# Optimization experiments

Measured on AMD Instinct MI355X. Metric: run time of the kernel, lower is better.

The kernel has to match this reference:

```python
import jax, jax.numpy as jnp
import numpy as np

B, S, D, H = 2, 2048, 1024, 16
DK = D // H


def setup_inputs() -> dict:
    key = jax.random.key(0)
    ks = jax.random.split(key, 12)
    s = 0.02
    return {
        "q": jax.random.normal(ks[0], (B, S, D), jnp.float32),
        "k": jax.random.normal(ks[1], (B, S, D), jnp.float32),
        "v": jax.random.normal(ks[2], (B, S, D), jnp.float32),
        "mask": jax.random.randint(ks[3], (1, 1, S, S), 0, 2, jnp.int32),
        "Wq": jax.random.normal(ks[4], (D, D), jnp.float32) * s,
        "bq": jnp.zeros((D,), jnp.float32),
        "Wk": jax.random.normal(ks[5], (D, D), jnp.float32) * s,
        "bk": jnp.zeros((D,), jnp.float32),
        "Wv": jax.random.normal(ks[6], (D, D), jnp.float32) * s,
        "bv": jnp.zeros((D,), jnp.float32),
        "Wo": jax.random.normal(ks[7], (D, D), jnp.float32) * s,
        "bo": jnp.zeros((D,), jnp.float32),
    }


def reference(q, k, v, mask, Wq, bq, Wk, bk, Wv, bv, Wo, bo):
    # linear projections (torch Linear: x @ W.T + b)
    qp = q @ Wq.T + bq
    kp = k @ Wk.T + bk
    vp = v @ Wv.T + bv
    # [B, S, D] -> [B, H, S, DK]
    split = lambda x: x.reshape(B, S, H, DK).transpose(0, 2, 1, 3)
    qh, kh, vh = split(qp), split(kp), split(vp)
    scale = 1.0 / jnp.sqrt(jnp.float32(DK))
    attn = jnp.einsum('bhsd,bhtd->bhst', qh, kh) * scale  # [B,H,S,S]
    attn = jnp.where(mask == 0, jnp.float32(-1e9), attn)
    attn = jax.nn.softmax(attn, axis=-1)
    out = jnp.einsum('bhst,bhtd->bhsd', attn, vh)  # [B,H,S,DK]
    concat = out.transpose(0, 2, 1, 3).reshape(B, S, D)
    return concat @ Wo.T + bo
```

## Files before the change

### kernel.cpp

```cpp
#include <hip/hip_runtime.h>
#include <hip/hip_bf16.h>


using bf16x8 = __attribute__((ext_vector_type(8))) short;
using f32x4  = __attribute__((ext_vector_type(4))) float;

constexpr int Bc = 2, Sc = 2048, Dc = 1024, Hc = 16, DKc = 64;
constexpr int Mc = Bc * Sc;
#define QSCALE 0.18033688011112042f

__device__ __forceinline__ void lds_load16(const void* g, void* l) {
  __builtin_amdgcn_global_load_lds(
      (const __attribute__((address_space(1))) unsigned int*)g,
      (__attribute__((address_space(3))) unsigned int*)l, 16, 0, 0);
}

#if __has_builtin(__builtin_amdgcn_exp2f)
__device__ __forceinline__ float exp2_fast(float x) { return __builtin_amdgcn_exp2f(x); }
#else
__device__ __forceinline__ float exp2_fast(float x) {
  float r;
  asm("v_exp_f32 %0, %1\n\ts_nop 0" : "=v"(r) : "v"(x));
  return r;
}
#endif

__device__ __forceinline__ unsigned pack_trunc(float a, float b) {
  return __builtin_amdgcn_perm(__float_as_uint(b), __float_as_uint(a), 0x07060302u);
}

__device__ __forceinline__ unsigned pack2bf(float a, float b) {
  union { __hip_bfloat16 h; unsigned short s; } ua, ub;
  ua.h = __float2bfloat16(a);
  ub.h = __float2bfloat16(b);
  return (unsigned)ua.s | ((unsigned)ub.s << 16);
}

__global__ void prep(const float* __restrict__ q, const float* __restrict__ k,
                     const float* __restrict__ v, const int* __restrict__ mask,
                     const float* __restrict__ Wq, const float* __restrict__ Wk,
                     const float* __restrict__ Wv, const float* __restrict__ Wo,
                     char* __restrict__ ws) {
  const size_t MB = 1024 * 1024;
  int blk = blockIdx.x;
  if (blk < 12288) {
    int which = blk >> 12;
    int i = (((blk & 4095) << 8) + threadIdx.x) * 4;
    const float* s = which == 0 ? q : (which == 1 ? k : v);
    __hip_bfloat16* d = (__hip_bfloat16*)(ws + (size_t)which * 8 * MB);
    float4 x = *(const float4*)&s[i];
    uint2 pk = {pack2bf(x.x, x.y), pack2bf(x.z, x.w)};
    *(uint2*)&d[i] = pk;
  } else if (blk < 16384) {
    int bb = blk - 12288;
    int which = bb >> 10;
    int i = (((bb & 1023) << 8) + threadIdx.x) * 4;
    const float* s = which == 0 ? Wq : (which == 1 ? Wk : (which == 2 ? Wv : Wo));
    __hip_bfloat16* d = which < 3 ? (__hip_bfloat16*)(ws + (24 + 2 * which) * MB)
                                  : (__hip_bfloat16*)(ws + 32 * MB);
    float4 x = *(const float4*)&s[i];
    uint2 pk = {pack2bf(x.x, x.y), pack2bf(x.z, x.w)};
    *(uint2*)&d[i] = pk;
  } else {
    int i = ((blk - 16384) << 8) + threadIdx.x;
    unsigned long long bal = __ballot(mask[i] != 0);
    if ((threadIdx.x & 63) == 0)
      ((unsigned long long*)(ws + 34 * MB))[i >> 6] = bal;
  }
}

__global__ __launch_bounds__(256, 3) void proj_qkv(
    const __hip_bfloat16* __restrict__ qb, const __hip_bfloat16* __restrict__ kb,
    const __hip_bfloat16* __restrict__ vb, const __hip_bfloat16* __restrict__ Wcat,
    const float* __restrict__ bq, const float* __restrict__ bk,
    const float* __restrict__ bv, __hip_bfloat16* __restrict__ qhd,
    __hip_bfloat16* __restrict__ khd, __hip_bfloat16* __restrict__ vtd) {
  __shared__ __align__(16) __hip_bfloat16 As[128 * 64];
  __shared__ __align__(16) __hip_bfloat16 Bs[128 * 64];
  const int tid = threadIdx.x;
  const int f = blockIdx.x, g = f >> 3;
  const int m0 = ((f & 7) * 4 + g / 24) * 128;
  const int n0 = (g % 24) * 128;
  const int which = n0 >> 10, nl0 = n0 & 1023;
  const __hip_bfloat16* X = which == 0 ? qb : (which == 1 ? kb : vb);
  const float* bias = which == 0 ? bq : (which == 1 ? bk : bv);
  const int w = tid >> 6, lane = tid & 63, ln = lane & 15, quad = lane >> 4;
  const int swz = ((lane & 7) ^ (lane >> 3)) * 8;
  const int rk0 = ln * 128 + ((quad ^ (ln & 7)) * 16);
  const int rk1 = ln * 128 + (((quad + 4) ^ (ln & 7)) * 16);
  const int aoff = (m0 + w * 32 + (lane >> 3)) * 1024 + swz;
  const int boff = (n0 + w * 32 + (lane >> 3)) * 1024 + swz;
  char* aF = (char*)As + (w >> 1) * 8192;
  char* bF = (char*)Bs + (w & 1) * 8192;
  char* aDst = (char*)As + w * 4096 + lane * 16;
  char* bDst = (char*)Bs + w * 4096 + lane * 16;
  f32x4 acc[4][4] = {};
  int ko = 0;
  for (int kb64 = 0; kb64 < 16; ++kb64, ko += 64) {
#pragma unroll
    for (int i = 0; i < 4; ++i) {
      lds_load16(&X[aoff + i * 8192 + ko], aDst + i * 1024);
      lds_load16(&Wcat[boff + i * 8192 + ko], bDst + i * 1024);
    }
    __syncthreads();
    bf16x8 af[4][2], bf[4][2];
#pragma unroll
    for (int i = 0; i < 4; ++i) {
      af[i][0] = *(bf16x8*)(aF + i * 2048 + rk0);
      af[i][1] = *(bf16x8*)(aF + i * 2048 + rk1);
      bf[i][0] = *(bf16x8*)(bF + i * 2048 + rk0);
      bf[i][1] = *(bf16x8*)(bF + i * 2048 + rk1);
    }
#pragma unroll
    for (int i = 0; i < 4; ++i)
#pragma unroll
      for (int j = 0; j < 4; ++j) {
        acc[i][j] = __builtin_amdgcn_mfma_f32_16x16x32_bf16(af[i][0], bf[j][0],
                                                            acc[i][j], 0, 0, 0);
        acc[i][j] = __builtin_amdgcn_mfma_f32_16x16x32_bf16(af[i][1], bf[j][1],
                                                            acc[i][j], 0, 0, 0);
      }
    __syncthreads();
  }
  const int wm = (w >> 1) * 64, wn = (w & 1) * 64;
#pragma unroll
  for (int i = 0; i < 4; ++i)
#pragma unroll
    for (int j = 0; j < 4; ++j) {
      int ngl = nl0 + wn + j * 16 + ln;
      int mbase = m0 + wm + i * 16 + quad * 4;
      float bb = bias[ngl];
      float vv[4];
#pragma unroll
      for (int r = 0; r < 4; ++r) vv[r] = acc[i][j][r] + bb;
      int h = ngl >> 6, dk = ngl & 63;
      int b = mbase >> 11, s = mbase & 2047;
      if (which == 0) {
#pragma unroll
        for (int r = 0; r < 4; ++r)
          qhd[(((size_t)(b * Hc + h) * Sc + s + r) * DKc) + dk] =
              __float2bfloat16(vv[r] * QSCALE);
      } else if (which == 1) {
#pragma unroll
        for (int r = 0; r < 4; ++r)
          khd[(((size_t)(b * Hc + h) * Sc + s + r) * DKc) + dk] =
              __float2bfloat16(vv[r]);
      } else {
        uint2 pk = {pack2bf(vv[0], vv[1]), pack2bf(vv[2], vv[3])};
        *(uint2*)&vtd[(((size_t)(b * Hc + h) * DKc + dk) * Sc) + s] = pk;
      }
    }
}

__global__ __launch_bounds__(256, 2) void gemm_out(
    const __hip_bfloat16* __restrict__ X, const __hip_bfloat16* __restrict__ W,
    const float* __restrict__ bias, float* __restrict__ Y) {
  __shared__ __align__(16) __hip_bfloat16 As[2][128 * 64];
  __shared__ __align__(16) __hip_bfloat16 Bs[2][64 * 64];
  const int tid = threadIdx.x;
  const int f = blockIdx.x, g = f >> 3;
  const int m0 = ((f & 7) * 4 + (g >> 4)) * 128;
  const int n0 = (g & 15) * 64;
  const int w = tid >> 6, lane = tid & 63, ln = lane & 15, quad = lane >> 4;
  const int wm = (w >> 1) * 64, wn = (w & 1) * 32;
  const int swz = ((lane & 7) ^ (lane >> 3)) * 8;
  const int rk0 = ln * 128 + ((quad ^ (ln & 7)) * 16);
  const int rk1 = ln * 128 + (((quad + 4) ^ (ln & 7)) * 16);
  const int aoff = (m0 + w * 32 + (lane >> 3)) * 1024 + swz;
  const int boff = (n0 + w * 16 + (lane >> 3)) * 1024 + swz;
  f32x4 acc[4][2] = {};

#define OSTAGE(KO, BI)                                                        \
  {                                                                           \
    _Pragma("unroll") for (int i = 0; i < 4; ++i)                             \
        lds_load16(&X[aoff + i * 8192 + (KO)],                                \
                   (char*)As[BI] + w * 4096 + lane * 16 + i * 1024);          \
    _Pragma("unroll") for (int i = 0; i < 2; ++i)                             \
        lds_load16(&W[boff + i * 8192 + (KO)],                                \
                   (char*)Bs[BI] + w * 2048 + lane * 16 + i * 1024);          \
  }

  OSTAGE(0, 0);
  for (int kb64 = 0; kb64 < 16; ++kb64) {
    const int bi = kb64 & 1;
    __syncthreads();
    if (kb64 + 1 < 16) OSTAGE((kb64 + 1) * 64, bi ^ 1);
    bf16x8 af[4][2], bf[2][2];
#pragma unroll
    for (int i = 0; i < 4; ++i) {
      af[i][0] = *(bf16x8*)((char*)As[bi] + wm * 128 + i * 2048 + rk0);
      af[i][1] = *(bf16x8*)((char*)As[bi] + wm * 128 + i * 2048 + rk1);
    }
#pragma unroll
    for (int j = 0; j < 2; ++j) {
      bf[j][0] = *(bf16x8*)((char*)Bs[bi] + wn * 128 + j * 2048 + rk0);
      bf[j][1] = *(bf16x8*)((char*)Bs[bi] + wn * 128 + j * 2048 + rk1);
    }
#pragma unroll
    for (int i = 0; i < 4; ++i)
#pragma unroll
      for (int j = 0; j < 2; ++j) {
        acc[i][j] = __builtin_amdgcn_mfma_f32_16x16x32_bf16(af[i][0], bf[j][0],
                                                            acc[i][j], 0, 0, 0);
        acc[i][j] = __builtin_amdgcn_mfma_f32_16x16x32_bf16(af[i][1], bf[j][1],
                                                            acc[i][j], 0, 0, 0);
      }
  }
#pragma unroll
  for (int i = 0; i < 4; ++i)
#pragma unroll
    for (int j = 0; j < 2; ++j) {
      int ng = n0 + wn + j * 16 + ln;
      int mbase = m0 + wm + i * 16 + quad * 4;
      float bb = bias[ng];
#pragma unroll
      for (int r = 0; r < 4; ++r)
        Y[(size_t)(mbase + r) * Dc + ng] = acc[i][j][r] + bb;
    }
}

__global__ __launch_bounds__(256, 3) void flash_attn(
    const __hip_bfloat16* __restrict__ qh, const __hip_bfloat16* __restrict__ kh,
    const __hip_bfloat16* __restrict__ vt, const uint4* __restrict__ mb4,
    float* __restrict__ opart, float* __restrict__ lpart) {
  __shared__ __align__(16) char L[51200];
  const int tid = threadIdx.x;
  const int f = blockIdx.x, g = f >> 3;
  const int bhh = (f & 7) * 8 + (g >> 4);
  const int q0 = (g & 15) * 128;
  const int half = bhh >> 5, bh = bhh & 31;
  const int w = tid >> 6, lane = tid & 63, ln = lane & 15, quad = lane >> 4;
  const size_t base = (size_t)bh * Sc * DKc;
  const __hip_bfloat16* khb = kh + base + half * 65536;
  const __hip_bfloat16* vtb = vt + base;

  bf16x8 qf[2][2];
#pragma unroll
  for (int qt = 0; qt < 2; ++qt)
#pragma unroll
    for (int kc = 0; kc < 2; ++kc)
      qf[qt][kc] = *(const bf16x8*)&qh[base +
          (size_t)(q0 + w * 32 + qt * 16 + ln) * 64 + kc * 32 + quad * 8];

  bf16x8 onesA;
#pragma unroll
  for (int i = 0; i < 8; ++i) onesA[i] = (short)0x3F80;

  const int swz = ((lane & 7) ^ (lane >> 3)) * 8;
  const int rk0 = ln * 128 + ((quad ^ (ln & 7)) * 16);
  const int rk1 = ln * 128 + (((quad + 4) ^ (ln & 7)) * 16);
  const int rPw = 32768 + w * 4608 + ln * 144 + quad * 8;
  const int rPb = 32768 + w * 4608 + ln * 144 + quad * 16;
  char* dmaL = L + w * 2048 + lane * 16;
  int koff = (w * 16 + (lane >> 3)) * 64 + swz;
  int voff0 = (w * 16 + (lane >> 3)) * Sc + swz + half * 1024;
  int voff1 = voff0 + 8 * Sc;
  int midx0 = (q0 + w * 32 + ln) * 16 + half * 8;
  int midx1 = midx0 + 256;
  const int sh0 = quad * 4, sh1 = quad * 4 + 16;

#define KV_DMA(BI)                                                            \
  {                                                                           \
    lds_load16(khb + koff, dmaL + (BI)*8192);                                 \
    lds_load16(khb + koff + 512, dmaL + (BI)*8192 + 1024);                    \
    lds_load16(vtb + voff0, dmaL + 16384 + (BI)*8192);                        \
    lds_load16(vtb + voff1, dmaL + 16384 + (BI)*8192 + 1024);                 \
  }

  f32x4 Oacc[4][2] = {};
  f32x4 lacc[2] = {};
  KV_DMA(0);

#define FTILE(BUF, LO0, HI0, LO1, HI1)                                        \
  {                                                                           \
    bf16x8 kf[4][2];                                                          \
    _Pragma("unroll") for (int tt = 0; tt < 4; ++tt) {                        \
      kf[tt][0] = *(bf16x8*)(L + (BUF)*8192 + tt * 2048 + rk0);               \
      kf[tt][1] = *(bf16x8*)(L + (BUF)*8192 + tt * 2048 + rk1);               \
    }                                                                         \
    _Pragma("unroll") for (int qt = 0; qt < 2; ++qt) {                        \
      f32x4 s[4];                                                             \
      _Pragma("unroll") for (int tt = 0; tt < 4; ++tt) {                      \
        f32x4 z = {0.f, 0.f, 0.f, 0.f};                                       \
        z = __builtin_amdgcn_mfma_f32_16x16x32_bf16(kf[tt][0], qf[qt][0], z,  \
                                                    0, 0, 0);                 \
        s[tt] = __builtin_amdgcn_mfma_f32_16x16x32_bf16(kf[tt][1], qf[qt][1], \
                                                        z, 0, 0, 0);          \
      }                                                                       \
      unsigned lo = qt ? (LO1) : (LO0), hi = qt ? (HI1) : (HI0);              \
      _Pragma("unroll") for (int tt = 0; tt < 4; ++tt) {                      \
        unsigned word = (tt & 2) ? hi : lo;                                   \
        unsigned pre = word >> ((tt & 1) ? sh1 : sh0);                        \
        float p[4];                                                           \
        _Pragma("unroll") for (int r = 0; r < 4; ++r) {                       \
          float e = exp2_fast(s[tt][r]);                                      \
          p[r] = (pre & (1u << r)) ? e : 0.f;                                 \
        }                                                                     \
        uint2 pk = {pack_trunc(p[0], p[1]), pack_trunc(p[2], p[3])};          \
        *(uint2*)(L + rPw + qt * 2304 + tt * 32) = pk;                        \
      }                                                                       \
    }                                                                         \
    bf16x8 vf[4][2], pb[2][2];                                                \
    _Pragma("unroll") for (int dt = 0; dt < 4; ++dt) {                        \
      vf[dt][0] = *(bf16x8*)(L + 16384 + (BUF)*8192 + dt * 2048 + rk0);       \
      vf[dt][1] = *(bf16x8*)(L + 16384 + (BUF)*8192 + dt * 2048 + rk1);       \
    }                                                                         \
    _Pragma("unroll") for (int qt = 0; qt < 2; ++qt) {                        \
      pb[qt][0] = *(bf16x8*)(L + rPb + qt * 2304);                            \
      pb[qt][1] = *(bf16x8*)(L + rPb + qt * 2304 + 64);                       \
    }                                                                         \
    _Pragma("unroll") for (int qt = 0; qt < 2; ++qt) {                        \
      lacc[qt] = __builtin_amdgcn_mfma_f32_16x16x32_bf16(onesA, pb[qt][0],    \
                                                         lacc[qt], 0, 0, 0);  \
      lacc[qt] = __builtin_amdgcn_mfma_f32_16x16x32_bf16(onesA, pb[qt][1],    \
                                                         lacc[qt], 0, 0, 0);  \
    }                                                                         \
    _Pragma("unroll") for (int dt = 0; dt < 4; ++dt)                          \
        _Pragma("unroll") for (int qt = 0; qt < 2; ++qt) {                    \
      Oacc[dt][qt] = __builtin_amdgcn_mfma_f32_16x16x32_bf16(                 \
          vf[dt][0], pb[qt][0], Oacc[dt][qt], 0, 0, 0);                       \
      Oacc[dt][qt] = __builtin_amdgcn_mfma_f32_16x16x32_bf16(                 \
          vf[dt][1], pb[qt][1], Oacc[dt][qt], 0, 0, 0);                       \
    }                                                                         \
  }

  for (int it2 = 0; it2 < 8; ++it2) {
    __syncthreads();
    uint4 mq0 = mb4[midx0], mq1 = mb4[midx1];
    ++midx0; ++midx1;
    koff += 4096; voff0 += 64; voff1 += 64;
    KV_DMA(1);
    FTILE(0, mq0.x, mq0.y, mq1.x, mq1.y);
    __syncthreads();
    if (it2 < 7) {
      koff += 4096; voff0 += 64; voff1 += 64;
      KV_DMA(0);
    }
    FTILE(1, mq0.z, mq0.w, mq1.z, mq1.w);
  }

  const size_t obase = (size_t)(half * 32 + bh) * 2048;
#pragma unroll
  for (int qt = 0; qt < 2; ++qt) {
    int qrow = q0 + w * 32 + qt * 16 + ln;
#pragma unroll
    for (int dt = 0; dt < 4; ++dt) {
      f32x4 o = Oacc[dt][qt];
      float4 st = {o[0], o[1], o[2], o[3]};
      *(float4*)&opart[(obase + qrow) * 64 + dt * 16 + quad * 4] = st;
    }
    if (quad == 0) lpart[obase + qrow] = lacc[qt][0];
  }
}

__global__ void reduce_o(const float* __restrict__ opart,
                         const float* __restrict__ lpart,
                         __hip_bfloat16* __restrict__ oc) {
  int t = blockIdx.x * 256 + threadIdx.x;
  int r = t >> 3, dk8 = (t & 7) * 8;
  const size_t HS = (size_t)32 * 2048 * 64;
  float4 a0 = *(const float4*)&opart[(size_t)r * 64 + dk8];
  float4 a1 = *(const float4*)&opart[(size_t)r * 64 + dk8 + 4];
  float4 b0 = *(const float4*)&opart[HS + (size_t)r * 64 + dk8];
  float4 b1 = *(const float4*)&opart[HS + (size_t)r * 64 + dk8 + 4];
  float li = 1.f / fmaxf(lpart[r] + lpart[65536 + r], 1e-30f);
  int bh = r >> 11, qq = r & 2047, b = bh >> 4, h = bh & 15;
  uint4 o;
  o.x = pack2bf((a0.x + b0.x) * li, (a0.y + b0.y) * li);
  o.y = pack2bf((a0.z + b0.z) * li, (a0.w + b0.w) * li);
  o.z = pack2bf((a1.x + b1.x) * li, (a1.y + b1.y) * li);
  o.w = pack2bf((a1.z + b1.z) * li, (a1.w + b1.w) * li);
  *(uint4*)&oc[((size_t)(b * Sc + qq) * Dc) + h * 64 + dk8] = o;
}

extern "C" void kernel_launch(void* const* d_in, const int* in_sizes, int n_in,
                              void* d_out, int out_size, void* d_ws, size_t ws_size,
                              hipStream_t stream) {
  const float* q  = (const float*)d_in[0];
  const float* k  = (const float*)d_in[1];
  const float* v  = (const float*)d_in[2];
  const int* mask = (const int*)d_in[3];
  const float* Wq = (const float*)d_in[4];
  const float* bq = (const float*)d_in[5];
  const float* Wk = (const float*)d_in[6];
  const float* bk = (const float*)d_in[7];
  const float* Wv = (const float*)d_in[8];
  const float* bv = (const float*)d_in[9];
  const float* Wo = (const float*)d_in[10];
  const float* bo = (const float*)d_in[11];

  char* ws = (char*)d_ws;
  const size_t MB = 1024 * 1024;
  __hip_bfloat16* qb   = (__hip_bfloat16*)(ws + 0 * MB);
  __hip_bfloat16* kb   = (__hip_bfloat16*)(ws + 8 * MB);
  __hip_bfloat16* vb   = (__hip_bfloat16*)(ws + 16 * MB);
  __hip_bfloat16* Wcat = (__hip_bfloat16*)(ws + 24 * MB);
  float*          opart = (float*)(ws + 0 * MB);
  __hip_bfloat16* Wob  = (__hip_bfloat16*)(ws + 32 * MB);
  uint4*          mb4  = (uint4*)(ws + 34 * MB);
  float*          lpart = (float*)(ws + 34 * MB + 512 * 1024);
  __hip_bfloat16* qhd  = (__hip_bfloat16*)(ws + 35 * MB);
  __hip_bfloat16* oc   = (__hip_bfloat16*)(ws + 35 * MB);
  __hip_bfloat16* khd  = (__hip_bfloat16*)(ws + 43 * MB);
  __hip_bfloat16* vtd  = (__hip_bfloat16*)(ws + 51 * MB);

  prep<<<32768, 256, 0, stream>>>(q, k, v, mask, Wq, Wk, Wv, Wo, ws);
  proj_qkv<<<768, 256, 0, stream>>>(qb, kb, vb, Wcat, bq, bk, bv, qhd, khd, vtd);
  flash_attn<<<1024, 256, 0, stream>>>(qhd, khd, vtd, mb4, opart, lpart);
  reduce_o<<<2048, 256, 0, stream>>>(opart, lpart, oc);
  gemm_out<<<512, 256, 0, stream>>>(oc, Wob, bo, (float*)d_out);
}
```

Baseline: 245.4 us.

## Drop split-KV attention with reduce kernel; normalize in-kernel and swap GEMM operands

```diff
diff --git a/kernel.cpp b/kernel.cpp
--- a/kernel.cpp
+++ b/kernel.cpp
@@ -57,7 +57,7 @@
     int i = (((bb & 1023) << 8) + threadIdx.x) * 4;
     const float* s = which == 0 ? Wq : (which == 1 ? Wk : (which == 2 ? Wv : Wo));
     __hip_bfloat16* d = which < 3 ? (__hip_bfloat16*)(ws + (24 + 2 * which) * MB)
-                                  : (__hip_bfloat16*)(ws + 32 * MB);
+                                  : (__hip_bfloat16*)(ws + 30 * MB);
     float4 x = *(const float4*)&s[i];
     uint2 pk = {pack2bf(x.x, x.y), pack2bf(x.z, x.w)};
     *(uint2*)&d[i] = pk;
@@ -65,7 +65,7 @@
     int i = ((blk - 16384) << 8) + threadIdx.x;
     unsigned long long bal = __ballot(mask[i] != 0);
     if ((threadIdx.x & 63) == 0)
-      ((unsigned long long*)(ws + 34 * MB))[i >> 6] = bal;
+      ((unsigned long long*)(ws + 32 * MB))[i >> 6] = bal;
   }
 }
 
@@ -88,8 +88,8 @@
   const int swz = ((lane & 7) ^ (lane >> 3)) * 8;
   const int rk0 = ln * 128 + ((quad ^ (ln & 7)) * 16);
   const int rk1 = ln * 128 + (((quad + 4) ^ (ln & 7)) * 16);
-  const int aoff = (m0 + w * 32 + (lane >> 3)) * 1024 + swz;
-  const int boff = (n0 + w * 32 + (lane >> 3)) * 1024 + swz;
+  const int aoff = (n0 + w * 32 + (lane >> 3)) * 1024 + swz;
+  const int boff = (m0 + w * 32 + (lane >> 3)) * 1024 + swz;
   char* aF = (char*)As + (w >> 1) * 8192;
   char* bF = (char*)Bs + (w & 1) * 8192;
   char* aDst = (char*)As + w * 4096 + lane * 16;
@@ -99,8 +99,8 @@
   for (int kb64 = 0; kb64 < 16; ++kb64, ko += 64) {
 #pragma unroll
     for (int i = 0; i < 4; ++i) {
-      lds_load16(&X[aoff + i * 8192 + ko], aDst + i * 1024);
-      lds_load16(&Wcat[boff + i * 8192 + ko], bDst + i * 1024);
+      lds_load16(&Wcat[aoff + i * 8192 + ko], aDst + i * 1024);
+      lds_load16(&X[boff + i * 8192 + ko], bDst + i * 1024);
     }
     __syncthreads();
     bf16x8 af[4][2], bf[4][2];
@@ -122,62 +122,61 @@
       }
     __syncthreads();
   }
-  const int wm = (w >> 1) * 64, wn = (w & 1) * 64;
-#pragma unroll
-  for (int i = 0; i < 4; ++i)
+  const int wA = (w >> 1) * 64, wB = (w & 1) * 64;
+#pragma unroll
+  for (int i = 0; i < 4; ++i) {
+    int nfb = nl0 + wA + i * 16 + quad * 4;
+    float4 b4 = *(const float4*)&bias[nfb];
+    int h = nfb >> 6, dk0 = nfb & 63;
 #pragma unroll
     for (int j = 0; j < 4; ++j) {
-      int ngl = nl0 + wn + j * 16 + ln;
-      int mbase = m0 + wm + i * 16 + quad * 4;
-      float bb = bias[ngl];
-      float vv[4];
-#pragma unroll
-      for (int r = 0; r < 4; ++r) vv[r] = acc[i][j][r] + bb;
-      int h = ngl >> 6, dk = ngl & 63;
-      int b = mbase >> 11, s = mbase & 2047;
+      int sg = m0 + wB + j * 16 + ln;
+      int b = sg >> 11, s = sg & 2047;
+      float vv[4] = {acc[i][j][0] + b4.x, acc[i][j][1] + b4.y,
+                     acc[i][j][2] + b4.z, acc[i][j][3] + b4.w};
       if (which == 0) {
+        uint2 pk = {pack2bf(vv[0] * QSCALE, vv[1] * QSCALE),
+                    pack2bf(vv[2] * QSCALE, vv[3] * QSCALE)};
+        *(uint2*)&qhd[(((size_t)(b * Hc + h) * Sc + s) * DKc) + dk0] = pk;
+      } else if (which == 1) {
+        uint2 pk = {pack2bf(vv[0], vv[1]), pack2bf(vv[2], vv[3])};
+        *(uint2*)&khd[(((size_t)(b * Hc + h) * Sc + s) * DKc) + dk0] = pk;
+      } else {
 #pragma unroll
         for (int r = 0; r < 4; ++r)
-          qhd[(((size_t)(b * Hc + h) * Sc + s + r) * DKc) + dk] =
-              __float2bfloat16(vv[r] * QSCALE);
-      } else if (which == 1) {
-#pragma unroll
-        for (int r = 0; r < 4; ++r)
-          khd[(((size_t)(b * Hc + h) * Sc + s + r) * DKc) + dk] =
+          vtd[(((size_t)(b * Hc + h) * DKc + dk0 + r) * Sc) + s] =
               __float2bfloat16(vv[r]);
-      } else {
-        uint2 pk = {pack2bf(vv[0], vv[1]), pack2bf(vv[2], vv[3])};
-        *(uint2*)&vtd[(((size_t)(b * Hc + h) * DKc + dk) * Sc) + s] = pk;
       }
     }
+  }
 }
 
 __global__ __launch_bounds__(256, 2) void gemm_out(
     const __hip_bfloat16* __restrict__ X, const __hip_bfloat16* __restrict__ W,
     const float* __restrict__ bias, float* __restrict__ Y) {
-  __shared__ __align__(16) __hip_bfloat16 As[2][128 * 64];
-  __shared__ __align__(16) __hip_bfloat16 Bs[2][64 * 64];
+  __shared__ __align__(16) __hip_bfloat16 As[2][64 * 64];
+  __shared__ __align__(16) __hip_bfloat16 Bs[2][128 * 64];
   const int tid = threadIdx.x;
   const int f = blockIdx.x, g = f >> 3;
   const int m0 = ((f & 7) * 4 + (g >> 4)) * 128;
   const int n0 = (g & 15) * 64;
   const int w = tid >> 6, lane = tid & 63, ln = lane & 15, quad = lane >> 4;
-  const int wm = (w >> 1) * 64, wn = (w & 1) * 32;
+  const int wA = (w & 1) * 32, wB = (w >> 1) * 64;
   const int swz = ((lane & 7) ^ (lane >> 3)) * 8;
   const int rk0 = ln * 128 + ((quad ^ (ln & 7)) * 16);
   const int rk1 = ln * 128 + (((quad + 4) ^ (ln & 7)) * 16);
-  const int aoff = (m0 + w * 32 + (lane >> 3)) * 1024 + swz;
-  const int boff = (n0 + w * 16 + (lane >> 3)) * 1024 + swz;
-  f32x4 acc[4][2] = {};
+  const int aoff = (n0 + w * 16 + (lane >> 3)) * 1024 + swz;
+  const int boff = (m0 + w * 32 + (lane >> 3)) * 1024 + swz;
+  f32x4 acc[2][4] = {};
 
 #define OSTAGE(KO, BI)                                                        \
   {                                                                           \
+    _Pragma("unroll") for (int i = 0; i < 2; ++i)                             \
+        lds_load16(&W[aoff + i * 8192 + (KO)],                                \
+                   (char*)As[BI] + w * 2048 + lane * 16 + i * 1024);          \
     _Pragma("unroll") for (int i = 0; i < 4; ++i)                             \
-        lds_load16(&X[aoff + i * 8192 + (KO)],                                \
-                   (char*)As[BI] + w * 4096 + lane * 16 + i * 1024);          \
-    _Pragma("unroll") for (int i = 0; i < 2; ++i)                             \
-        lds_load16(&W[boff + i * 8192 + (KO)],                                \
-                   (char*)Bs[BI] + w * 2048 + lane * 16 + i * 1024);          \
+        lds_load16(&X[boff + i * 8192 + (KO)],                                \
+                   (char*)Bs[BI] + w * 4096 + lane * 16 + i * 1024);          \
   }
 
   OSTAGE(0, 0);
@@ -185,21 +184,21 @@
     const int bi = kb64 & 1;
     __syncthreads();
     if (kb64 + 1 < 16) OSTAGE((kb64 + 1) * 64, bi ^ 1);
-    bf16x8 af[4][2], bf[2][2];
-#pragma unroll
-    for (int i = 0; i < 4; ++i) {
-      af[i][0] = *(bf16x8*)((char*)As[bi] + wm * 128 + i * 2048 + rk0);
-      af[i][1] = *(bf16x8*)((char*)As[bi] + wm * 128 + i * 2048 + rk1);
-    }
-#pragma unroll
-    for (int j = 0; j < 2; ++j) {
-      bf[j][0] = *(bf16x8*)((char*)Bs[bi] + wn * 128 + j * 2048 + rk0);
-      bf[j][1] = *(bf16x8*)((char*)Bs[bi] + wn * 128 + j * 2048 + rk1);
-    }
-#pragma unroll
-    for (int i = 0; i < 4; ++i)
-#pragma unroll
-      for (int j = 0; j < 2; ++j) {
+    bf16x8 af[2][2], bf[4][2];
+#pragma unroll
+    for (int i = 0; i < 2; ++i) {
+      af[i][0] = *(bf16x8*)((char*)As[bi] + wA * 128 + i * 2048 + rk0);
+      af[i][1] = *(bf16x8*)((char*)As[bi] + wA * 128 + i * 2048 + rk1);
+    }
+#pragma unroll
+    for (int j = 0; j < 4; ++j) {
+      bf[j][0] = *(bf16x8*)((char*)Bs[bi] + wB * 128 + j * 2048 + rk0);
+      bf[j][1] = *(bf16x8*)((char*)Bs[bi] + wB * 128 + j * 2048 + rk1);
+    }
+#pragma unroll
+    for (int i = 0; i < 2; ++i)
+#pragma unroll
+      for (int j = 0; j < 4; ++j) {
         acc[i][j] = __builtin_amdgcn_mfma_f32_16x16x32_bf16(af[i][0], bf[j][0],
                                                             acc[i][j], 0, 0, 0);
         acc[i][j] = __builtin_amdgcn_mfma_f32_16x16x32_bf16(af[i][1], bf[j][1],
@@ -207,31 +206,32 @@
       }
   }
 #pragma unroll
-  for (int i = 0; i < 4; ++i)
-#pragma unroll
-    for (int j = 0; j < 2; ++j) {
-      int ng = n0 + wn + j * 16 + ln;
-      int mbase = m0 + wm + i * 16 + quad * 4;
-      float bb = bias[ng];
-#pragma unroll
-      for (int r = 0; r < 4; ++r)
-        Y[(size_t)(mbase + r) * Dc + ng] = acc[i][j][r] + bb;
-    }
+  for (int i = 0; i < 2; ++i) {
+    int nfb = n0 + wA + i * 16 + quad * 4;
+    float4 b4 = *(const float4*)&bias[nfb];
+#pragma unroll
+    for (int j = 0; j < 4; ++j) {
+      int sg = m0 + wB + j * 16 + ln;
+      float4 st = {acc[i][j][0] + b4.x, acc[i][j][1] + b4.y,
+                   acc[i][j][2] + b4.z, acc[i][j][3] + b4.w};
+      *(float4*)&Y[(size_t)sg * Dc + nfb] = st;
+    }
+  }
 }
 
 __global__ __launch_bounds__(256, 3) void flash_attn(
     const __hip_bfloat16* __restrict__ qh, const __hip_bfloat16* __restrict__ kh,
     const __hip_bfloat16* __restrict__ vt, const uint4* __restrict__ mb4,
-    float* __restrict__ opart, float* __restrict__ lpart) {
+    __hip_bfloat16* __restrict__ oc) {
   __shared__ __align__(16) char L[51200];
   const int tid = threadIdx.x;
   const int f = blockIdx.x, g = f >> 3;
-  const int bhh = (f & 7) * 8 + (g >> 4);
+  const int bh = (f & 7) * 4 + (g >> 4);
   const int q0 = (g & 15) * 128;
-  const int half = bhh >> 5, bh = bhh & 31;
+  const int b = bh >> 4, h = bh & 15;
   const int w = tid >> 6, lane = tid & 63, ln = lane & 15, quad = lane >> 4;
   const size_t base = (size_t)bh * Sc * DKc;
-  const __hip_bfloat16* khb = kh + base + half * 65536;
+  const __hip_bfloat16* khb = kh + base;
   const __hip_bfloat16* vtb = vt + base;
 
   bf16x8 qf[2][2];
@@ -253,9 +253,9 @@
   const int rPb = 32768 + w * 4608 + ln * 144 + quad * 16;
   char* dmaL = L + w * 2048 + lane * 16;
   int koff = (w * 16 + (lane >> 3)) * 64 + swz;
-  int voff0 = (w * 16 + (lane >> 3)) * Sc + swz + half * 1024;
+  int voff0 = (w * 16 + (lane >> 3)) * Sc + swz;
   int voff1 = voff0 + 8 * Sc;
-  int midx0 = (q0 + w * 32 + ln) * 16 + half * 8;
+  int midx0 = (q0 + w * 32 + ln) * 16;
   int midx1 = midx0 + 256;
   const int sh0 = quad * 4, sh1 = quad * 4 + 16;
 
@@ -324,7 +324,7 @@
     }                                                                         \
   }
 
-  for (int it2 = 0; it2 < 8; ++it2) {
+  for (int it2 = 0; it2 < 16; ++it2) {
     __syncthreads();
     uint4 mq0 = mb4[midx0], mq1 = mb4[midx1];
     ++midx0; ++midx1;
@@ -332,45 +332,34 @@
     KV_DMA(1);
     FTILE(0, mq0.x, mq0.y, mq1.x, mq1.y);
     __syncthreads();
-    if (it2 < 7) {
+    if (it2 < 15) {
       koff += 4096; voff0 += 64; voff1 += 64;
       KV_DMA(0);
     }
     FTILE(1, mq0.z, mq0.w, mq1.z, mq1.w);
   }
 
-  const size_t obase = (size_t)(half * 32 + bh) * 2048;
-#pragma unroll
-  for (int qt = 0; qt < 2; ++qt) {
-    int qrow = q0 + w * 32 + qt * 16 + ln;
-#pragma unroll
-    for (int dt = 0; dt < 4; ++dt) {
+  float linv[2];
+#pragma unroll
+  for (int qt = 0; qt < 2; ++qt)
+    linv[qt] = 1.f / fmaxf(lacc[qt][0], 1e-30f);
+#pragma unroll
+  for (int dt = 0; dt < 4; ++dt)
+#pragma unroll
+    for (int qt = 0; qt < 2; ++qt) {
       f32x4 o = Oacc[dt][qt];
-      float4 st = {o[0], o[1], o[2], o[3]};
-      *(float4*)&opart[(obase + qrow) * 64 + dt * 16 + quad * 4] = st;
-    }
-    if (quad == 0) lpart[obase + qrow] = lacc[qt][0];
-  }
-}
-
-__global__ void reduce_o(const float* __restrict__ opart,
-                         const float* __restrict__ lpart,
-                         __hip_bfloat16* __restrict__ oc) {
-  int t = blockIdx.x * 256 + threadIdx.x;
-  int r = t >> 3, dk8 = (t & 7) * 8;
-  const size_t HS = (size_t)32 * 2048 * 64;
-  float4 a0 = *(const float4*)&opart[(size_t)r * 64 + dk8];
-  float4 a1 = *(const float4*)&opart[(size_t)r * 64 + dk8 + 4];
-  float4 b0 = *(const float4*)&opart[HS + (size_t)r * 64 + dk8];
-  float4 b1 = *(const float4*)&opart[HS + (size_t)r * 64 + dk8 + 4];
-  float li = 1.f / fmaxf(lpart[r] + lpart[65536 + r], 1e-30f);
-  int bh = r >> 11, qq = r & 2047, b = bh >> 4, h = bh & 15;
-  uint4 o;
-  o.x = pack2bf((a0.x + b0.x) * li, (a0.y + b0.y) * li);
-  o.y = pack2bf((a0.z + b0.z) * li, (a0.w + b0.w) * li);
-  o.z = pack2bf((a1.x + b1.x) * li, (a1.y + b1.y) * li);
-  o.w = pack2bf((a1.z + b1.z) * li, (a1.w + b1.w) * li);
-  *(uint4*)&oc[((size_t)(b * Sc + qq) * Dc) + h * 64 + dk8] = o;
+      uint2 pk = {pack2bf(o[0] * linv[qt], o[1] * linv[qt]),
+                  pack2bf(o[2] * linv[qt], o[3] * linv[qt])};
+      *(uint2*)(L + rPw + qt * 2304 + dt * 32) = pk;
+    }
+  __builtin_amdgcn_s_waitcnt(0);
+#pragma unroll
+  for (int chunk = 0; chunk < 4; ++chunk) {
+    int row = chunk * 8 + (lane >> 3);
+    bf16x8 val = *(bf16x8*)(L + 32768 + w * 4608 + row * 144 + (lane & 7) * 16);
+    int s = q0 + w * 32 + row;
+    *(bf16x8*)&oc[(size_t)(b * Sc + s) * Dc + h * 64 + (lane & 7) * 8] = val;
+  }
 }
 
 extern "C" void kernel_launch(void* const* d_in, const int* in_sizes, int n_in,
@@ -395,18 +384,15 @@
   __hip_bfloat16* kb   = (__hip_bfloat16*)(ws + 8 * MB);
   __hip_bfloat16* vb   = (__hip_bfloat16*)(ws + 16 * MB);
   __hip_bfloat16* Wcat = (__hip_bfloat16*)(ws + 24 * MB);
-  float*          opart = (float*)(ws + 0 * MB);
-  __hip_bfloat16* Wob  = (__hip_bfloat16*)(ws + 32 * MB);
-  uint4*          mb4  = (uint4*)(ws + 34 * MB);
-  float*          lpart = (float*)(ws + 34 * MB + 512 * 1024);
-  __hip_bfloat16* qhd  = (__hip_bfloat16*)(ws + 35 * MB);
-  __hip_bfloat16* oc   = (__hip_bfloat16*)(ws + 35 * MB);
-  __hip_bfloat16* khd  = (__hip_bfloat16*)(ws + 43 * MB);
-  __hip_bfloat16* vtd  = (__hip_bfloat16*)(ws + 51 * MB);
+  __hip_bfloat16* Wob  = (__hip_bfloat16*)(ws + 30 * MB);
+  uint4*          mb4  = (uint4*)(ws + 32 * MB);
+  __hip_bfloat16* qhd  = (__hip_bfloat16*)(ws + 33 * MB);
+  __hip_bfloat16* khd  = (__hip_bfloat16*)(ws + 41 * MB);
+  __hip_bfloat16* vtd  = (__hip_bfloat16*)(ws + 49 * MB);
+  __hip_bfloat16* oc   = (__hip_bfloat16*)(ws + 57 * MB);
 
   prep<<<32768, 256, 0, stream>>>(q, k, v, mask, Wq, Wk, Wv, Wo, ws);
   proj_qkv<<<768, 256, 0, stream>>>(qb, kb, vb, Wcat, bq, bk, bv, qhd, khd, vtd);
-  flash_attn<<<1024, 256, 0, stream>>>(qhd, khd, vtd, mb4, opart, lpart);
-  reduce_o<<<2048, 256, 0, stream>>>(opart, lpart, oc);
+  flash_attn<<<512, 256, 0, stream>>>(qhd, khd, vtd, mb4, oc);
   gemm_out<<<512, 256, 0, stream>>>(oc, Wob, bo, (float*)d_out);
 }
```

After: 246.8 us. No clear change (+0.6%).
